# Kernel tuning notes

Measured on AMD Instinct MI355X. Metric: run time of the kernel, lower is better.

## Reference

```python
import jax, jax.numpy as jnp
import numpy as np

N = 20000          # nodes
E = 320000         # edges (before self loops)
NG = 16            # graphs in batch
DIN = 256          # input_dim = heads*hidden
HID = 64           # hidden_dim
HEADS = 4
EPS = 1e-5         # LayerNorm eps
SLOPE = 0.2        # GATConv leaky_relu negative slope


def _ln(x, g, b):
    mu = jnp.mean(x, -1, keepdims=True)
    var = jnp.mean((x - mu) ** 2, -1, keepdims=True)
    return (x - mu) * jax.lax.rsqrt(var + EPS) * g + b


def _gat(x, src, dst, W, a_src, a_dst, bias, heads, out_dim, concat):
    # x: [N, F]; W: [F, heads*out_dim]; a_src/a_dst: [heads, out_dim]
    h = (x @ W).reshape(-1, heads, out_dim)              # [N, H, D]
    e_s = jnp.sum(h * a_src, -1)                         # [N, H]
    e_d = jnp.sum(h * a_dst, -1)                         # [N, H]
    e = jax.nn.leaky_relu(e_s[src] + e_d[dst], SLOPE)    # [E, H]
    # segment softmax over edges sharing the same target node
    m = jax.ops.segment_max(e, dst, num_segments=N)
    m = jnp.where(jnp.isfinite(m), m, 0.0)
    ex = jnp.exp(e - m[dst])
    s = jax.ops.segment_sum(ex, dst, num_segments=N)
    alpha = ex / (s[dst] + 1e-16)                        # [E, H]
    out = jax.ops.segment_sum(h[src] * alpha[:, :, None], dst, num_segments=N)
    out = out.reshape(-1, heads * out_dim) if concat else out.mean(1)
    return out + bias


def setup_inputs() -> dict:
    key = jax.random.key(0)
    ks = jax.random.split(key, 24)
    sc = 0.05
    inp = {
        "node_x": jax.random.normal(ks[0], (N, DIN), dtype=jnp.float32),
        "edge_index": jax.random.randint(ks[1], (2, E), 0, N, dtype=jnp.int64),
        "batch": jnp.sort(jax.random.randint(ks[2], (N,), 0, NG, dtype=jnp.int64)),
        # layer 1 (concat, heads=4)
        "W1": jax.random.normal(ks[3], (DIN, HEADS * HID), dtype=jnp.float32) * sc,
        "as1": jax.random.normal(ks[4], (HEADS, HID), dtype=jnp.float32) * sc,
        "ad1": jax.random.normal(ks[5], (HEADS, HID), dtype=jnp.float32) * sc,
        "b1": jnp.zeros((HEADS * HID,), dtype=jnp.float32),
        "g1": jnp.ones((HEADS * HID,), dtype=jnp.float32),
        "be1": jnp.zeros((HEADS * HID,), dtype=jnp.float32),
        # layer 2 (concat, heads=4)
        "W2": jax.random.normal(ks[6], (HEADS * HID, HEADS * HID), dtype=jnp.float32) * sc,
        "as2": jax.random.normal(ks[7], (HEADS, HID), dtype=jnp.float32) * sc,
        "ad2": jax.random.normal(ks[8], (HEADS, HID), dtype=jnp.float32) * sc,
        "b2": jnp.zeros((HEADS * HID,), dtype=jnp.float32),
        "g2": jnp.ones((HEADS * HID,), dtype=jnp.float32),
        "be2": jnp.zeros((HEADS * HID,), dtype=jnp.float32),
        # final (heads=1, averaged)
        "Wf": jax.random.normal(ks[9], (HEADS * HID, HID), dtype=jnp.float32) * sc,
        "asf": jax.random.normal(ks[10], (1, HID), dtype=jnp.float32) * sc,
        "adf": jax.random.normal(ks[11], (1, HID), dtype=jnp.float32) * sc,
        "bf": jnp.zeros((HID,), dtype=jnp.float32),
        "gf": jnp.ones((HID,), dtype=jnp.float32),
        "bef": jnp.zeros((HID,), dtype=jnp.float32),
    }
    return inp


def reference(node_x, edge_index, batch, W1, as1, ad1, b1, g1, be1,
              W2, as2, ad2, b2, g2, be2, Wf, asf, adf, bf, gf, bef):
    loops = jnp.arange(N, dtype=edge_index.dtype)
    src = jnp.concatenate([edge_index[0], loops])   # PyG add_self_loops=True
    dst = jnp.concatenate([edge_index[1], loops])

    x = node_x
    # layer 1 + LN + relu + residual (shapes match: DIN == HEADS*HID)
    r = x
    x = _gat(x, src, dst, W1, as1, ad1, b1, HEADS, HID, True)
    x = jax.nn.relu(_ln(x, g1, be1)) + r
    # layer 2
    r = x
    x = _gat(x, src, dst, W2, as2, ad2, b2, HEADS, HID, True)
    x = jax.nn.relu(_ln(x, g2, be2)) + r
    # final layer (heads=1, mean over heads), LN then relu
    x = _gat(x, src, dst, Wf, asf, adf, bf, 1, HID, False)
    x = jax.nn.relu(_ln(x, gf, bef))

    counts = jax.ops.segment_sum(jnp.ones((N,), x.dtype), batch, num_segments=NG)
    mean = jax.ops.segment_sum(x, batch, num_segments=NG) / jnp.clip(counts, 1.0)[:, None]
    mx = jax.ops.segment_max(x, batch, num_segments=NG)
    mx = jnp.where(jnp.isfinite(mx), mx, 0.0)
    pooled = jnp.concatenate([mean, mx], -1)
    return (x, pooled)
```

## Files before the change

### kernel.cpp

```cpp
#include <hip/hip_runtime.h>
#include <cstdint>
#include <cstddef>

#define NN 20000
#define EE 320000
#define TE (EE + NN)
#define NG 16
#define HEADS 4
#define LN_EPS 1e-5f
#define SLOPE 0.2f

typedef __attribute__((ext_vector_type(8))) short bfx8;
typedef __attribute__((ext_vector_type(8))) unsigned short u16x8;
typedef __attribute__((ext_vector_type(4))) float f32x4;
typedef __attribute__((ext_vector_type(8))) float f32x8;

__device__ __forceinline__ short f2bf(float f) {
    unsigned u = __float_as_uint(f);
    u += 0x7FFFu + ((u >> 16) & 1u);
    return (short)(u >> 16);
}
__device__ __forceinline__ float bf2f(unsigned short u) {
    return __uint_as_float(((unsigned)u) << 16);
}
__device__ __forceinline__ float lrelu(float e) {
    return (e >= 0.f) ? e : SLOPE * e;
}

__global__ void deg_kernel(const int* __restrict__ ei, int* __restrict__ counts) {
    int i = blockIdx.x * blockDim.x + threadIdx.x;
    if (i >= TE) return;
    int d = (i < EE) ? ei[EE + i] : (i - EE);
    atomicAdd(&counts[d], 1);
}

__global__ __launch_bounds__(256) void bsum_kernel(const int* __restrict__ cnt,
                                                   int* __restrict__ bsum) {
    int b = blockIdx.x;
    int i = b * 256 + threadIdx.x;
    int v = (i < NN) ? cnt[i] : 0;
    for (int s = 32; s > 0; s >>= 1) v += __shfl_down(v, s);
    __shared__ int ws4[4];
    int lane = threadIdx.x & 63, w = threadIdx.x >> 6;
    if (lane == 0) ws4[w] = v;
    __syncthreads();
    if (threadIdx.x == 0) bsum[b] = ws4[0] + ws4[1] + ws4[2] + ws4[3];
}

__global__ void bscan_kernel(const int* __restrict__ bsum, int* __restrict__ boff, int nb) {
    __shared__ int s[128];
    int t = threadIdx.x;
    int v = (t < nb) ? bsum[t] : 0;
    s[t] = v;
    __syncthreads();
    for (int st = 1; st < 128; st <<= 1) {
        int a = (t >= st) ? s[t - st] : 0;
        __syncthreads();
        s[t] += a;
        __syncthreads();
    }
    if (t < nb) boff[t] = s[t] - v;
}

__global__ __launch_bounds__(256) void offsets_kernel(const int* __restrict__ cnt,
                                                      const int* __restrict__ boff,
                                                      int* __restrict__ off,
                                                      int* __restrict__ cursor) {
    int b = blockIdx.x, t = threadIdx.x;
    int i = b * 256 + t;
    int v = (i < NN) ? cnt[i] : 0;
    int lane = t & 63, w = t >> 6;
    int x = v;
    for (int s = 1; s < 64; s <<= 1) {
        int u = __shfl_up(x, s);
        if (lane >= s) x += u;
    }
    __shared__ int wsum[4];
    if (lane == 63) wsum[w] = x;
    __syncthreads();
    int pre = 0;
    for (int k = 0; k < w; k++) pre += wsum[k];
    int excl = (x + pre - v) + boff[b];
    if (i < NN) { cursor[i] = excl; off[i] = excl; }
    if (i == NN - 1) off[NN] = excl + v;
}

__global__ void csr_fill_kernel(const int* __restrict__ ei, int* __restrict__ cursor,
                                int* __restrict__ csr_src, int* __restrict__ csr_dst) {
    int i = blockIdx.x * blockDim.x + threadIdx.x;
    if (i >= TE) return;
    int s, d;
    if (i < EE) { s = ei[i]; d = ei[EE + i]; }
    else        { s = i - EE; d = s; }
    int pos = atomicAdd(&cursor[d], 1);
    csr_src[pos] = s;
    csr_dst[pos] = d;
}

__global__ void gstart_kernel(const int* __restrict__ batch, int* __restrict__ gstart) {
    int g = threadIdx.x;
    if (g > NG) return;
    int lo = 0, hi = NN;
    while (lo < hi) {
        int mid = (lo + hi) >> 1;
        if (batch[mid] < g) lo = mid + 1; else hi = mid;
    }
    gstart[g] = lo;
}

__global__ void cvt_bf16_kernel(const float* __restrict__ in, unsigned short* __restrict__ out, int n4) {
    int i = blockIdx.x * blockDim.x + threadIdx.x;
    if (i >= n4) return;
    float4 v = ((const float4*)in)[i];
    ushort4 o;
    o.x = f2bf(v.x); o.y = f2bf(v.y); o.z = f2bf(v.z); o.w = f2bf(v.w);
    ((ushort4*)out)[i] = o;
}

__global__ __launch_bounds__(256) void transpose_cvt_kernel(const float* __restrict__ W,
                                                            short* __restrict__ WT,
                                                            int K, int Nc) {
    __shared__ float tile[32][33];
    int bx = blockIdx.x * 32;
    int by = blockIdx.y * 32;
    int tx = threadIdx.x & 31, ty = threadIdx.x >> 5;
    for (int r = ty; r < 32; r += 8)
        tile[r][tx] = W[(size_t)(by + r) * Nc + bx + tx];
    __syncthreads();
    for (int r = ty; r < 32; r += 8)
        WT[(size_t)(bx + r) * K + by + tx] = f2bf(tile[tx][r]);
}

#define GBM 64
#define GBN 64
#define GBK 64
__global__ __launch_bounds__(256) void gemm_attn_kernel(const short* __restrict__ A,
                                                        const short* __restrict__ BT,
                                                        unsigned short* __restrict__ Cb,
                                                        float* __restrict__ es,
                                                        float* __restrict__ ed,
                                                        const float* __restrict__ av_src,
                                                        const float* __restrict__ av_dst,
                                                        int M, int K, int Nc, int nheads) {
    __shared__ short Al[GBM * GBK];
    __shared__ short Bl[GBN * GBK];
    __shared__ float sps[64][2];
    __shared__ float spd[64][2];
    const int t = threadIdx.x;
    const int lane = t & 63, wid = t >> 6;
    const int wr = (wid >> 1) * 32, wc = (wid & 1) * 32;
    const int bm = blockIdx.x * GBM, bn = blockIdx.y * GBN;
    const int r0 = t >> 3, ch = t & 7;

    f32x4 acc[2][2] = {};

    for (int k0 = 0; k0 < K; k0 += GBK) {
#pragma unroll
        for (int p = 0; p < 2; p++) {
            int row = p * 32 + r0;
            int arow = bm + row; if (arow >= M) arow = M - 1;
            bfx8 av = *(const bfx8*)(A + (size_t)arow * K + k0 + ch * 8);
            bfx8 bv = *(const bfx8*)(BT + (size_t)(bn + row) * K + k0 + ch * 8);
            int wo = (row << 7) + (((ch ^ (row & 7))) << 4);
            *(bfx8*)((char*)Al + wo) = av;
            *(bfx8*)((char*)Bl + wo) = bv;
        }
        __syncthreads();
        bfx8 af[2][2], bfm[2][2];
#pragma unroll
        for (int m = 0; m < 2; m++)
#pragma unroll
            for (int kk = 0; kk < 2; kk++) {
                int rowa = wr + m * 16 + (lane & 15);
                int rowb = wc + m * 16 + (lane & 15);
                int c = kk * 4 + (lane >> 4);
                af[m][kk]  = *(const bfx8*)((const char*)Al + (rowa << 7) + (((c ^ (rowa & 7))) << 4));
                bfm[m][kk] = *(const bfx8*)((const char*)Bl + (rowb << 7) + (((c ^ (rowb & 7))) << 4));
            }
#pragma unroll
        for (int m = 0; m < 2; m++)
#pragma unroll
            for (int n = 0; n < 2; n++) {
                acc[m][n] = __builtin_amdgcn_mfma_f32_16x16x32_bf16(af[m][0], bfm[n][0], acc[m][n], 0, 0, 0);
                acc[m][n] = __builtin_amdgcn_mfma_f32_16x16x32_bf16(af[m][1], bfm[n][1], acc[m][n], 0, 0, 0);
            }
        __syncthreads();
    }

#pragma unroll
    for (int m = 0; m < 2; m++) {
        int row0 = bm + wr + m * 16 + ((lane >> 4) << 2);
#pragma unroll
        for (int n = 0; n < 2; n++) {
            int col = bn + wc + n * 16 + (lane & 15);
#pragma unroll
            for (int j = 0; j < 4; j++) {
                int row = row0 + j;
                if (row < M) Cb[(size_t)row * Nc + col] = (unsigned short)f2bf(acc[m][n][j]);
            }
        }
    }

    const int hd = bn >> 6;
    float asv[2], adv[2];
#pragma unroll
    for (int n = 0; n < 2; n++) {
        int c = wc + n * 16 + (lane & 15);
        asv[n] = av_src[hd * 64 + c];
        adv[n] = av_dst[hd * 64 + c];
    }
#pragma unroll
    for (int m = 0; m < 2; m++) {
#pragma unroll
        for (int j = 0; j < 4; j++) {
            float ps = acc[m][0][j] * asv[0] + acc[m][1][j] * asv[1];
            float pd = acc[m][0][j] * adv[0] + acc[m][1][j] * adv[1];
            ps += __shfl_xor(ps, 1); pd += __shfl_xor(pd, 1);
            ps += __shfl_xor(ps, 2); pd += __shfl_xor(pd, 2);
            ps += __shfl_xor(ps, 4); pd += __shfl_xor(pd, 4);
            ps += __shfl_xor(ps, 8); pd += __shfl_xor(pd, 8);
            if ((lane & 15) == 0) {
                int rl = wr + m * 16 + ((lane >> 4) << 2) + j;
                sps[rl][wid & 1] = ps;
                spd[rl][wid & 1] = pd;
            }
        }
    }
    __syncthreads();
    if (t < 64) {
        int row = bm + t;
        if (row < M) {
            es[(size_t)row * nheads + hd] = sps[t][0] + sps[t][1];
            ed[(size_t)row * nheads + hd] = spd[t][0] + spd[t][1];
        }
    }
}

__global__ void wexp4_kernel(const int* __restrict__ csrs, const int* __restrict__ csrd,
                             const float* __restrict__ es, const float* __restrict__ ed,
                             float* __restrict__ wbuf) {
    int i = blockIdx.x * blockDim.x + threadIdx.x;
    if (i >= TE) return;
    int s = csrs[i], d = csrd[i];
    float4 a = ((const float4*)es)[s];
    float4 b = ((const float4*)ed)[d];
    float4 o;
    o.x = __expf(lrelu(a.x + b.x));
    o.y = __expf(lrelu(a.y + b.y));
    o.z = __expf(lrelu(a.z + b.z));
    o.w = __expf(lrelu(a.w + b.w));
    ((float4*)wbuf)[i] = o;
}

__global__ void wexp1_kernel(const int* __restrict__ csrs, const int* __restrict__ csrd,
                             const float* __restrict__ es, const float* __restrict__ ed,
                             float* __restrict__ wbuf) {
    int i = blockIdx.x * blockDim.x + threadIdx.x;
    if (i >= TE) return;
    wbuf[i] = __expf(lrelu(es[csrs[i]] + ed[csrd[i]]));
}

__global__ __launch_bounds__(256) void gat_agg_ln_kernel(
    const unsigned short* __restrict__ hb, const float* __restrict__ wbuf,
    const int* __restrict__ off, const int* __restrict__ csrs,
    const float* __restrict__ bias, const float* __restrict__ gamma, const float* __restrict__ beta,
    const float* __restrict__ resid, float* __restrict__ xout, unsigned short* __restrict__ xbout) {
    const int wid = threadIdx.x >> 6, lane = threadIdx.x & 63;
    const int n = blockIdx.x * 4 + wid;
    const int half = lane >> 5, sl = lane & 31;
    const int hd = sl >> 3;
    const int d0 = sl * 8;
    const int j0 = off[n], j1 = off[n + 1];

    float acc[8] = {};
    float wsum = 0.f;
    int j = j0 + half;
    for (; j + 6 < j1; j += 8) {
        int s0 = csrs[j], s1 = csrs[j + 2], s2 = csrs[j + 4], s3 = csrs[j + 6];
        float w0 = wbuf[j * 4 + hd];
        float w1 = wbuf[(j + 2) * 4 + hd];
        float w2 = wbuf[(j + 4) * 4 + hd];
        float w3 = wbuf[(j + 6) * 4 + hd];
        u16x8 r0 = *(const u16x8*)(hb + (size_t)s0 * 256 + d0);
        u16x8 r1 = *(const u16x8*)(hb + (size_t)s1 * 256 + d0);
        u16x8 r2 = *(const u16x8*)(hb + (size_t)s2 * 256 + d0);
        u16x8 r3 = *(const u16x8*)(hb + (size_t)s3 * 256 + d0);
        wsum += (w0 + w1) + (w2 + w3);
#pragma unroll
        for (int k = 0; k < 8; k++)
            acc[k] += w0 * bf2f(r0[k]) + w1 * bf2f(r1[k]) + w2 * bf2f(r2[k]) + w3 * bf2f(r3[k]);
    }
    for (; j < j1; j += 2) {
        int s = csrs[j];
        float wt = wbuf[j * 4 + hd];
        u16x8 r = *(const u16x8*)(hb + (size_t)s * 256 + d0);
        wsum += wt;
#pragma unroll
        for (int k = 0; k < 8; k++) acc[k] += wt * bf2f(r[k]);
    }
    wsum += __shfl_xor(wsum, 32);
#pragma unroll
    for (int k = 0; k < 8; k++) acc[k] += __shfl_xor(acc[k], 32);

    float inv = 1.f / (wsum + 1e-16f);
    f32x8 bi = *(const f32x8*)(bias + d0);
    float v[8];
    float ls = 0.f, lq = 0.f;
#pragma unroll
    for (int k = 0; k < 8; k++) {
        v[k] = acc[k] * inv + bi[k];
        ls += v[k];
        lq += v[k] * v[k];
    }
    ls += __shfl_xor(ls, 1);  lq += __shfl_xor(lq, 1);
    ls += __shfl_xor(ls, 2);  lq += __shfl_xor(lq, 2);
    ls += __shfl_xor(ls, 4);  lq += __shfl_xor(lq, 4);
    ls += __shfl_xor(ls, 8);  lq += __shfl_xor(lq, 8);
    ls += __shfl_xor(ls, 16); lq += __shfl_xor(lq, 16);
    float mu = ls * (1.0f / 256.0f);
    float var = lq * (1.0f / 256.0f) - mu * mu;
    float rstd = rsqrtf(var + LN_EPS);
    f32x8 ga = *(const f32x8*)(gamma + d0);
    f32x8 be = *(const f32x8*)(beta + d0);
    f32x8 rs = {};
    if (half == 0) rs = *(const f32x8*)(resid + (size_t)n * 256 + d0);
    float y[8];
#pragma unroll
    for (int k = 0; k < 8; k++) {
        float yy = fmaxf((v[k] - mu) * rstd * ga[k] + be[k], 0.f) + rs[k];
        float tt = __shfl_xor(yy, 32);
        y[k] = half ? tt : yy;
    }
    if (half == 0) {
        if (xout) {
            f32x8 o;
#pragma unroll
            for (int k = 0; k < 8; k++) o[k] = y[k];
            *(f32x8*)(xout + (size_t)n * 256 + d0) = o;
        }
    } else {
        u16x8 ob;
#pragma unroll
        for (int k = 0; k < 8; k++) ob[k] = (unsigned short)f2bf(y[k]);
        *(u16x8*)(xbout + (size_t)n * 256 + d0) = ob;
    }
}

__global__ __launch_bounds__(256) void gat_final_kernel(
    const unsigned short* __restrict__ hb, const float* __restrict__ wf,
    const int* __restrict__ off, const int* __restrict__ csrs,
    const float* __restrict__ bias, const float* __restrict__ gamma, const float* __restrict__ beta,
    float* __restrict__ xout) {
    const int wid = threadIdx.x >> 6, lane = threadIdx.x & 63;
    const int n = blockIdx.x * 4 + wid;
    const int q = lane >> 4, sq = lane & 15;
    const int d0 = sq * 4;
    const int j0 = off[n], j1 = off[n + 1];

    float acc[4] = {};
    float wsum = 0.f;
    int j = j0 + q;
    for (; j + 4 < j1; j += 8) {
        int s0 = csrs[j], s1 = csrs[j + 4];
        float w0 = wf[j], w1 = wf[j + 4];
        ushort4 r0 = *(const ushort4*)(hb + (size_t)s0 * 64 + d0);
        ushort4 r1 = *(const ushort4*)(hb + (size_t)s1 * 64 + d0);
        wsum += w0 + w1;
        acc[0] += w0 * bf2f(r0.x) + w1 * bf2f(r1.x);
        acc[1] += w0 * bf2f(r0.y) + w1 * bf2f(r1.y);
        acc[2] += w0 * bf2f(r0.z) + w1 * bf2f(r1.z);
        acc[3] += w0 * bf2f(r0.w) + w1 * bf2f(r1.w);
    }
    for (; j < j1; j += 4) {
        int s = csrs[j];
        float wt = wf[j];
        ushort4 r = *(const ushort4*)(hb + (size_t)s * 64 + d0);
        wsum += wt;
        acc[0] += wt * bf2f(r.x);
        acc[1] += wt * bf2f(r.y);
        acc[2] += wt * bf2f(r.z);
        acc[3] += wt * bf2f(r.w);
    }
    wsum += __shfl_xor(wsum, 16);
    wsum += __shfl_xor(wsum, 32);
#pragma unroll
    for (int k = 0; k < 4; k++) {
        acc[k] += __shfl_xor(acc[k], 16);
        acc[k] += __shfl_xor(acc[k], 32);
    }
    float inv = 1.f / (wsum + 1e-16f);
    float4 bi = *(const float4*)(bias + d0);
    float v[4];
    float ls = 0.f, lq = 0.f;
    v[0] = acc[0] * inv + bi.x; v[1] = acc[1] * inv + bi.y;
    v[2] = acc[2] * inv + bi.z; v[3] = acc[3] * inv + bi.w;
#pragma unroll
    for (int k = 0; k < 4; k++) { ls += v[k]; lq += v[k] * v[k]; }
    ls += __shfl_xor(ls, 1); lq += __shfl_xor(lq, 1);
    ls += __shfl_xor(ls, 2); lq += __shfl_xor(lq, 2);
    ls += __shfl_xor(ls, 4); lq += __shfl_xor(lq, 4);
    ls += __shfl_xor(ls, 8); lq += __shfl_xor(lq, 8);
    float mu = ls * (1.0f / 64.0f);
    float var = lq * (1.0f / 64.0f) - mu * mu;
    float rstd = rsqrtf(var + LN_EPS);
    if (q == 0) {
        float4 ga = *(const float4*)(gamma + d0);
        float4 be = *(const float4*)(beta + d0);
        float4 o;
        o.x = fmaxf((v[0] - mu) * rstd * ga.x + be.x, 0.f);
        o.y = fmaxf((v[1] - mu) * rstd * ga.y + be.y, 0.f);
        o.z = fmaxf((v[2] - mu) * rstd * ga.z + be.z, 0.f);
        o.w = fmaxf((v[3] - mu) * rstd * ga.w + be.w, 0.f);
        *(float4*)(xout + (size_t)n * 64 + d0) = o;
    }
}

__global__ __launch_bounds__(256) void pool_partial_kernel(
    const float* __restrict__ x, const int* __restrict__ gstart,
    float* __restrict__ gsum, unsigned* __restrict__ gmax) {
    int g = blockIdx.x, sp = blockIdx.y;
    int r0 = gstart[g], r1 = gstart[g + 1];
    int t = threadIdx.x, d = t & 63, rg = t >> 6;
    float sum = 0.f, mx = 0.f;
    for (int r = r0 + sp * 4 + rg; r < r1; r += 32) {
        float v = x[(size_t)r * 64 + d];
        sum += v;
        mx = fmaxf(mx, v);
    }
    __shared__ float S[256], M[256];
    S[t] = sum; M[t] = mx;
    __syncthreads();
    if (t < 64) {
        float s4 = S[t] + S[t + 64] + S[t + 128] + S[t + 192];
        float m4 = fmaxf(fmaxf(M[t], M[t + 64]), fmaxf(M[t + 128], M[t + 192]));
        atomicAdd(&gsum[g * 64 + t], s4);
        atomicMax(&gmax[g * 64 + t], __float_as_uint(m4));
    }
}

__global__ void pool_final_kernel(const float* __restrict__ gsum,
                                  const unsigned* __restrict__ gmax,
                                  const int* __restrict__ gstart,
                                  float* __restrict__ pout) {
    int g = blockIdx.x, d = threadIdx.x;
    float c = fmaxf((float)(gstart[g + 1] - gstart[g]), 1.0f);
    pout[g * 128 + d] = gsum[g * 64 + d] / c;
    pout[g * 128 + 64 + d] = __uint_as_float(gmax[g * 64 + d]);
}

extern "C" void kernel_launch(void* const* d_in, const int* in_sizes, int n_in,
                              void* d_out, int out_size, void* d_ws, size_t ws_size,
                              hipStream_t stream) {
    const float* node_x = (const float*)d_in[0];
    const int*   ei     = (const int*)d_in[1];
    const int*   batch  = (const int*)d_in[2];
    const float* W1  = (const float*)d_in[3];
    const float* as1 = (const float*)d_in[4];
    const float* ad1 = (const float*)d_in[5];
    const float* b1  = (const float*)d_in[6];
    const float* g1  = (const float*)d_in[7];
    const float* be1 = (const float*)d_in[8];
    const float* W2  = (const float*)d_in[9];
    const float* as2 = (const float*)d_in[10];
    const float* ad2 = (const float*)d_in[11];
    const float* b2  = (const float*)d_in[12];
    const float* g2  = (const float*)d_in[13];
    const float* be2 = (const float*)d_in[14];
    const float* Wf  = (const float*)d_in[15];
    const float* asf = (const float*)d_in[16];
    const float* adf = (const float*)d_in[17];
    const float* bf  = (const float*)d_in[18];
    const float* gf  = (const float*)d_in[19];
    const float* bef = (const float*)d_in[20];
    float* out = (float*)d_out;

    char* w = (char*)d_ws;
    auto alloc = [&](size_t bytes) -> void* {
        void* p = (void*)w;
        w += (bytes + 255) & ~(size_t)255;
        return p;
    };
    unsigned short* hb   = (unsigned short*)alloc((size_t)NN * 256 * 2);
    float*          x1   = (float*)alloc((size_t)NN * 256 * 4);
    unsigned short* xb   = (unsigned short*)alloc((size_t)NN * 256 * 2);
    short*          wt   = (short*)alloc((size_t)256 * 256 * 2);
    float*          es   = (float*)alloc((size_t)NN * HEADS * 4);
    float*          ed   = (float*)alloc((size_t)NN * HEADS * 4);
    float*          wbuf = (float*)alloc((size_t)TE * HEADS * 4);
    int*      counts = (int*)alloc((size_t)NN * 4);
    int*      off    = (int*)alloc((size_t)(NN + 1) * 4);
    int*      cursor = (int*)alloc((size_t)NN * 4);
    int*      csrs   = (int*)alloc((size_t)TE * 4);
    int*      csrd   = (int*)alloc((size_t)TE * 4);
    int*      bsum   = (int*)alloc((size_t)128 * 4);
    int*      boff   = (int*)alloc((size_t)128 * 4);
    float*    gsum   = (float*)alloc((size_t)NG * 64 * 4);
    unsigned* gmax   = (unsigned*)alloc((size_t)NG * 64 * 4);
    int*      gstart = (int*)alloc((size_t)(NG + 1) * 4);

    hipMemsetAsync(counts, 0, (size_t)NN * 4, stream);
    hipMemsetAsync(gsum, 0, (size_t)NG * 64 * 4, stream);
    hipMemsetAsync(gmax, 0, (size_t)NG * 64 * 4, stream);

    const int NB = (NN + 255) / 256;
    const int EB = (TE + 255) / 256;

    deg_kernel<<<EB, 256, 0, stream>>>(ei, counts);
    bsum_kernel<<<NB, 256, 0, stream>>>(counts, bsum);
    bscan_kernel<<<1, 128, 0, stream>>>(bsum, boff, NB);
    offsets_kernel<<<NB, 256, 0, stream>>>(counts, boff, off, cursor);
    csr_fill_kernel<<<EB, 256, 0, stream>>>(ei, cursor, csrs, csrd);
    gstart_kernel<<<1, 32, 0, stream>>>(batch, gstart);

    const int n4 = NN * 256 / 4;
    dim3 tg256(8, 8), tg64(2, 8);
    dim3 gg256((NN + GBM - 1) / GBM, 256 / GBN);
    dim3 gg64((NN + GBM - 1) / GBM, 1);

    cvt_bf16_kernel<<<(n4 + 255) / 256, 256, 0, stream>>>(node_x, xb, n4);
    transpose_cvt_kernel<<<tg256, 256, 0, stream>>>(W1, wt, 256, 256);
    gemm_attn_kernel<<<gg256, 256, 0, stream>>>((const short*)xb, wt, hb, es, ed, as1, ad1, NN, 256, 256, HEADS);
    wexp4_kernel<<<EB, 256, 0, stream>>>(csrs, csrd, es, ed, wbuf);
    gat_agg_ln_kernel<<<NN / 4, 256, 0, stream>>>(hb, wbuf, off, csrs, b1, g1, be1, node_x, x1, xb);
    transpose_cvt_kernel<<<tg256, 256, 0, stream>>>(W2, wt, 256, 256);
    gemm_attn_kernel<<<gg256, 256, 0, stream>>>((const short*)xb, wt, hb, es, ed, as2, ad2, NN, 256, 256, HEADS);
    wexp4_kernel<<<EB, 256, 0, stream>>>(csrs, csrd, es, ed, wbuf);
    gat_agg_ln_kernel<<<NN / 4, 256, 0, stream>>>(hb, wbuf, off, csrs, b2, g2, be2, x1, nullptr, xb);
    transpose_cvt_kernel<<<tg64, 256, 0, stream>>>(Wf, wt, 256, 64);
    gemm_attn_kernel<<<gg64, 256, 0, stream>>>((const short*)xb, wt, hb, es, ed, asf, adf, NN, 256, 64, 1);
    wexp1_kernel<<<EB, 256, 0, stream>>>(csrs, csrd, es, ed, wbuf);
    gat_final_kernel<<<NN / 4, 256, 0, stream>>>(hb, wbuf, off, csrs, bf, gf, bef, out);
    pool_partial_kernel<<<dim3(NG, 8), 256, 0, stream>>>(out, gstart, gsum, gmax);
    pool_final_kernel<<<NG, 64, 0, stream>>>(gsum, gmax, gstart, out + (size_t)NN * 64);
}
```

Baseline: 302.5 us.

## Fuse edge softmax weights into aggregation kernels and drop fp32 residual buffer

Removes the separate per-edge exp kernels and the wbuf array. Each aggregation kernel now recomputes exp(leaky_relu(es[src]+ed[dst])) inline from the per-node attention scalars, and the csr_dst array is no longer written. The fp32 copy x1 of the layer-1 output is also dropped: layer 2 reads its residual from the bf16 buffer, using two ping-pong bf16 buffers. This saves several launches and large edge-sized memory traffic, at the cost of redundant exp work per lane and reduced residual precision in layer 2.

```diff
diff --git a/kernel.cpp b/kernel.cpp
--- a/kernel.cpp
+++ b/kernel.cpp
@@ -86,7 +86,7 @@
 }
 
 __global__ void csr_fill_kernel(const int* __restrict__ ei, int* __restrict__ cursor,
-                                int* __restrict__ csr_src, int* __restrict__ csr_dst) {
+                                int* __restrict__ csr_src) {
     int i = blockIdx.x * blockDim.x + threadIdx.x;
     if (i >= TE) return;
     int s, d;
@@ -94,7 +94,6 @@
     else        { s = i - EE; d = s; }
     int pos = atomicAdd(&cursor[d], 1);
     csr_src[pos] = s;
-    csr_dst[pos] = d;
 }
 
 __global__ void gstart_kernel(const int* __restrict__ batch, int* __restrict__ gstart) {
@@ -236,51 +235,30 @@
     }
 }
 
-__global__ void wexp4_kernel(const int* __restrict__ csrs, const int* __restrict__ csrd,
-                             const float* __restrict__ es, const float* __restrict__ ed,
-                             float* __restrict__ wbuf) {
-    int i = blockIdx.x * blockDim.x + threadIdx.x;
-    if (i >= TE) return;
-    int s = csrs[i], d = csrd[i];
-    float4 a = ((const float4*)es)[s];
-    float4 b = ((const float4*)ed)[d];
-    float4 o;
-    o.x = __expf(lrelu(a.x + b.x));
-    o.y = __expf(lrelu(a.y + b.y));
-    o.z = __expf(lrelu(a.z + b.z));
-    o.w = __expf(lrelu(a.w + b.w));
-    ((float4*)wbuf)[i] = o;
-}
-
-__global__ void wexp1_kernel(const int* __restrict__ csrs, const int* __restrict__ csrd,
-                             const float* __restrict__ es, const float* __restrict__ ed,
-                             float* __restrict__ wbuf) {
-    int i = blockIdx.x * blockDim.x + threadIdx.x;
-    if (i >= TE) return;
-    wbuf[i] = __expf(lrelu(es[csrs[i]] + ed[csrd[i]]));
-}
-
 __global__ __launch_bounds__(256) void gat_agg_ln_kernel(
-    const unsigned short* __restrict__ hb, const float* __restrict__ wbuf,
+    const unsigned short* __restrict__ hb,
+    const float* __restrict__ es, const float* __restrict__ ed,
     const int* __restrict__ off, const int* __restrict__ csrs,
     const float* __restrict__ bias, const float* __restrict__ gamma, const float* __restrict__ beta,
-    const float* __restrict__ resid, float* __restrict__ xout, unsigned short* __restrict__ xbout) {
+    const float* __restrict__ residf, const unsigned short* __restrict__ residb,
+    unsigned short* __restrict__ xbout) {
     const int wid = threadIdx.x >> 6, lane = threadIdx.x & 63;
     const int n = blockIdx.x * 4 + wid;
     const int half = lane >> 5, sl = lane & 31;
     const int hd = sl >> 3;
     const int d0 = sl * 8;
     const int j0 = off[n], j1 = off[n + 1];
+    const float edn = ed[n * HEADS + hd];
 
     float acc[8] = {};
     float wsum = 0.f;
     int j = j0 + half;
     for (; j + 6 < j1; j += 8) {
         int s0 = csrs[j], s1 = csrs[j + 2], s2 = csrs[j + 4], s3 = csrs[j + 6];
-        float w0 = wbuf[j * 4 + hd];
-        float w1 = wbuf[(j + 2) * 4 + hd];
-        float w2 = wbuf[(j + 4) * 4 + hd];
-        float w3 = wbuf[(j + 6) * 4 + hd];
+        float w0 = __expf(lrelu(es[s0 * HEADS + hd] + edn));
+        float w1 = __expf(lrelu(es[s1 * HEADS + hd] + edn));
+        float w2 = __expf(lrelu(es[s2 * HEADS + hd] + edn));
+        float w3 = __expf(lrelu(es[s3 * HEADS + hd] + edn));
         u16x8 r0 = *(const u16x8*)(hb + (size_t)s0 * 256 + d0);
         u16x8 r1 = *(const u16x8*)(hb + (size_t)s1 * 256 + d0);
         u16x8 r2 = *(const u16x8*)(hb + (size_t)s2 * 256 + d0);
@@ -292,7 +270,7 @@
     }
     for (; j < j1; j += 2) {
         int s = csrs[j];
-        float wt = wbuf[j * 4 + hd];
+        float wt = __expf(lrelu(es[s * HEADS + hd] + edn));
         u16x8 r = *(const u16x8*)(hb + (size_t)s * 256 + d0);
         wsum += wt;
 #pragma unroll
@@ -323,7 +301,15 @@
     f32x8 ga = *(const f32x8*)(gamma + d0);
     f32x8 be = *(const f32x8*)(beta + d0);
     f32x8 rs = {};
-    if (half == 0) rs = *(const f32x8*)(resid + (size_t)n * 256 + d0);
+    if (half == 0) {
+        if (residf) {
+            rs = *(const f32x8*)(residf + (size_t)n * 256 + d0);
+        } else {
+            u16x8 rb = *(const u16x8*)(residb + (size_t)n * 256 + d0);
+#pragma unroll
+            for (int k = 0; k < 8; k++) rs[k] = bf2f(rb[k]);
+        }
+    }
     float y[8];
 #pragma unroll
     for (int k = 0; k < 8; k++) {
@@ -331,14 +317,7 @@
         float tt = __shfl_xor(yy, 32);
         y[k] = half ? tt : yy;
     }
-    if (half == 0) {
-        if (xout) {
-            f32x8 o;
-#pragma unroll
-            for (int k = 0; k < 8; k++) o[k] = y[k];
-            *(f32x8*)(xout + (size_t)n * 256 + d0) = o;
-        }
-    } else {
+    if (half == 1) {
         u16x8 ob;
 #pragma unroll
         for (int k = 0; k < 8; k++) ob[k] = (unsigned short)f2bf(y[k]);
@@ -347,7 +326,8 @@
 }
 
 __global__ __launch_bounds__(256) void gat_final_kernel(
-    const unsigned short* __restrict__ hb, const float* __restrict__ wf,
+    const unsigned short* __restrict__ hb,
+    const float* __restrict__ es, const float* __restrict__ ed,
     const int* __restrict__ off, const int* __restrict__ csrs,
     const float* __restrict__ bias, const float* __restrict__ gamma, const float* __restrict__ beta,
     float* __restrict__ xout) {
@@ -356,13 +336,15 @@
     const int q = lane >> 4, sq = lane & 15;
     const int d0 = sq * 4;
     const int j0 = off[n], j1 = off[n + 1];
+    const float edn = ed[n];
 
     float acc[4] = {};
     float wsum = 0.f;
     int j = j0 + q;
     for (; j + 4 < j1; j += 8) {
         int s0 = csrs[j], s1 = csrs[j + 4];
-        float w0 = wf[j], w1 = wf[j + 4];
+        float w0 = __expf(lrelu(es[s0] + edn));
+        float w1 = __expf(lrelu(es[s1] + edn));
         ushort4 r0 = *(const ushort4*)(hb + (size_t)s0 * 64 + d0);
         ushort4 r1 = *(const ushort4*)(hb + (size_t)s1 * 64 + d0);
         wsum += w0 + w1;
@@ -373,7 +355,7 @@
     }
     for (; j < j1; j += 4) {
         int s = csrs[j];
-        float wt = wf[j];
+        float wt = __expf(lrelu(es[s] + edn));
         ushort4 r = *(const ushort4*)(hb + (size_t)s * 64 + d0);
         wsum += wt;
         acc[0] += wt * bf2f(r.x);
@@ -481,17 +463,15 @@
         return p;
     };
     unsigned short* hb   = (unsigned short*)alloc((size_t)NN * 256 * 2);
-    float*          x1   = (float*)alloc((size_t)NN * 256 * 4);
-    unsigned short* xb   = (unsigned short*)alloc((size_t)NN * 256 * 2);
+    unsigned short* xbA  = (unsigned short*)alloc((size_t)NN * 256 * 2);
+    unsigned short* xbB  = (unsigned short*)alloc((size_t)NN * 256 * 2);
     short*          wt   = (short*)alloc((size_t)256 * 256 * 2);
     float*          es   = (float*)alloc((size_t)NN * HEADS * 4);
     float*          ed   = (float*)alloc((size_t)NN * HEADS * 4);
-    float*          wbuf = (float*)alloc((size_t)TE * HEADS * 4);
     int*      counts = (int*)alloc((size_t)NN * 4);
     int*      off    = (int*)alloc((size_t)(NN + 1) * 4);
     int*      cursor = (int*)alloc((size_t)NN * 4);
     int*      csrs   = (int*)alloc((size_t)TE * 4);
-    int*      csrd   = (int*)alloc((size_t)TE * 4);
     int*      bsum   = (int*)alloc((size_t)128 * 4);
     int*      boff   = (int*)alloc((size_t)128 * 4);
     float*    gsum   = (float*)alloc((size_t)NG * 64 * 4);
@@ -509,7 +489,7 @@
     bsum_kernel<<<NB, 256, 0, stream>>>(counts, bsum);
     bscan_kernel<<<1, 128, 0, stream>>>(bsum, boff, NB);
     offsets_kernel<<<NB, 256, 0, stream>>>(counts, boff, off, cursor);
-    csr_fill_kernel<<<EB, 256, 0, stream>>>(ei, cursor, csrs, csrd);
+    csr_fill_kernel<<<EB, 256, 0, stream>>>(ei, cursor, csrs);
     gstart_kernel<<<1, 32, 0, stream>>>(batch, gstart);
 
     const int n4 = NN * 256 / 4;
@@ -517,19 +497,16 @@
     dim3 gg256((NN + GBM - 1) / GBM, 256 / GBN);
     dim3 gg64((NN + GBM - 1) / GBM, 1);
 
-    cvt_bf16_kernel<<<(n4 + 255) / 256, 256, 0, stream>>>(node_x, xb, n4);
+    cvt_bf16_kernel<<<(n4 + 255) / 256, 256, 0, stream>>>(node_x, xbA, n4);
     transpose_cvt_kernel<<<tg256, 256, 0, stream>>>(W1, wt, 256, 256);
-    gemm_attn_kernel<<<gg256, 256, 0, stream>>>((const short*)xb, wt, hb, es, ed, as1, ad1, NN, 256, 256, HEADS);
-    wexp4_kernel<<<EB, 256, 0, stream>>>(csrs, csrd, es, ed, wbuf);
-    gat_agg_ln_kernel<<<NN / 4, 256, 0, stream>>>(hb, wbuf, off, csrs, b1, g1, be1, node_x, x1, xb);
+    gemm_attn_kernel<<<gg256, 256, 0, stream>>>((const short*)xbA, wt, hb, es, ed, as1, ad1, NN, 256, 256, HEADS);
+    gat_agg_ln_kernel<<<NN / 4, 256, 0, stream>>>(hb, es, ed, off, csrs, b1, g1, be1, node_x, nullptr, xbB);
     transpose_cvt_kernel<<<tg256, 256, 0, stream>>>(W2, wt, 256, 256);
-    gemm_attn_kernel<<<gg256, 256, 0, stream>>>((const short*)xb, wt, hb, es, ed, as2, ad2, NN, 256, 256, HEADS);
-    wexp4_kernel<<<EB, 256, 0, stream>>>(csrs, csrd, es, ed, wbuf);
-    gat_agg_ln_kernel<<<NN / 4, 256, 0, stream>>>(hb, wbuf, off, csrs, b2, g2, be2, x1, nullptr, xb);
+    gemm_attn_kernel<<<gg256, 256, 0, stream>>>((const short*)xbB, wt, hb, es, ed, as2, ad2, NN, 256, 256, HEADS);
+    gat_agg_ln_kernel<<<NN / 4, 256, 0, stream>>>(hb, es, ed, off, csrs, b2, g2, be2, nullptr, xbB, xbA);
     transpose_cvt_kernel<<<tg64, 256, 0, stream>>>(Wf, wt, 256, 64);
-    gemm_attn_kernel<<<gg64, 256, 0, stream>>>((const short*)xb, wt, hb, es, ed, asf, adf, NN, 256, 64, 1);
-    wexp1_kernel<<<EB, 256, 0, stream>>>(csrs, csrd, es, ed, wbuf);
-    gat_final_kernel<<<NN / 4, 256, 0, stream>>>(hb, wbuf, off, csrs, bf, gf, bef, out);
+    gemm_attn_kernel<<<gg64, 256, 0, stream>>>((const short*)xbA, wt, hb, es, ed, asf, adf, NN, 256, 64, 1);
+    gat_final_kernel<<<NN / 4, 256, 0, stream>>>(hb, es, ed, off, csrs, bf, gf, bef, out);
     pool_partial_kernel<<<dim3(NG, 8), 256, 0, stream>>>(out, gstart, gsum, gmax);
     pool_final_kernel<<<NG, 64, 0, stream>>>(gsum, gmax, gstart, out + (size_t)NN * 64);
 }
```

Result: faster. 283.1 us (-6.4%).
